# Performance work log

Measured on AMD Instinct MI355X. Metric: run time of the kernel, lower is better.

Reference implementation:

```python
import jax, jax.numpy as jnp
import numpy as np

B_IMG, T_PER, DIN = 8, 4096, 1176
D, E, BN, L, TOP_K, OUT = 1024, 8, 64, 4, 2, 4096


def setup_inputs() -> dict:
    key = jax.random.key(0)
    ks = jax.random.split(key, 16)
    s = 0.02
    inp = {
        "pixel_values": jax.random.normal(ks[0], (B_IMG * T_PER, DIN), jnp.float32),
        "image_grid_thw": jnp.tile(jnp.array([[1, 64, 64]], dtype=jnp.int64), (B_IMG, 1)),
        # in_proj (no bias)
        "w_in": jax.random.normal(ks[1], (DIN, D), jnp.float32) * s,
        # skin classifier: Linear(D,64) -> ReLU -> Linear(64,3)
        "w_sc1": jax.random.normal(ks[2], (D, 64), jnp.float32) * s,
        "b_sc1": jnp.zeros((64,), jnp.float32),
        "w_sc2": jax.random.normal(ks[3], (64, 3), jnp.float32) * s,
        "b_sc2": jnp.zeros((3,), jnp.float32),
        # per-adapter-layer routers (stacked over L)
        "w_rimg": jax.random.normal(ks[4], (L, D, E), jnp.float32) * s,
        "w_rskin": jax.random.normal(ks[5], (L, 3, E), jnp.float32) * s,
        # per-layer, per-expert MLP: Linear(D,BN) -> ReLU -> Linear(BN,D)
        "ew1": jax.random.normal(ks[6], (L, E, D, BN), jnp.float32) * s,
        "eb1": jnp.zeros((L, E, BN), jnp.float32),
        "ew2": jax.random.normal(ks[7], (L, E, BN, D), jnp.float32) * s,
        "eb2": jnp.zeros((L, E, D), jnp.float32),
        # out_proj
        "w_out": jax.random.normal(ks[8], (D, OUT), jnp.float32) * s,
        "b_out": jnp.zeros((OUT,), jnp.float32),
    }
    return inp


def _forward(pixel_values, image_grid_thw, w_in, w_sc1, b_sc1, w_sc2, b_sc2,
             w_rimg, w_rskin, ew1, eb1, ew2, eb2, w_out, b_out):
    B = image_grid_thw.shape[0]
    T = pixel_values.shape[0] // B  # equal chunk sizes (t*h*w identical per image)
    x = pixel_values.reshape(B, T, -1)

    def per_image(xc):  # xc: [T, din]
        h = xc @ w_in  # [T, D]
        g = h.mean(0)
        skin_logits = jax.nn.relu(g @ w_sc1 + b_sc1) @ w_sc2 + b_sc2  # [3]
        skin_probs = jax.nn.softmax(skin_logits)

        def layer(carry, params):
            h, aux = carry
            wri, wrs, W1, B1, W2, B2 = params
            logits = h @ wri + skin_probs @ wrs  # [T, E]
            probs = jax.nn.softmax(logits, axis=-1)
            tp, ti = jax.lax.top_k(probs, TOP_K)
            tp = tp / (tp.sum(-1, keepdims=True) + 1e-6)
            rows = jnp.arange(h.shape[0])[:, None]
            # dense per-token expert weights (0 for non-selected experts)
            wfull = jnp.zeros_like(probs).at[rows, ti].add(tp)
            mask = jnp.zeros_like(probs).at[rows, ti].add(1.0)
            h1 = jax.nn.relu(jnp.einsum('td,edb->teb', h, W1) + B1)  # [T,E,BN]
            h2 = jnp.einsum('teb,ebd->ted', h1, W2) + B2             # [T,E,D]
            moe_out = jnp.einsum('ted,te->td', h2, wfull)
            aux = aux + (probs.mean(0) * mask.mean(0)).sum() * probs.shape[-1]
            return (h + moe_out, aux), None

        (h, aux), _ = jax.lax.scan(layer, (h, jnp.zeros((), h.dtype)),
                                   (w_rimg, w_rskin, ew1, eb1, ew2, eb2))
        return h.mean(0), skin_logits, aux

    pooled, skin_logits, aux = jax.vmap(per_image)(x)
    vision_proj = pooled @ w_out + b_out
    return pooled, vision_proj, aux.sum(), skin_logits


def reference(pixel_values, image_grid_thw, w_in, w_sc1, b_sc1, w_sc2, b_sc2,
              w_rimg, w_rskin, ew1, eb1, ew2, eb2, w_out, b_out):
    return _forward(pixel_values, image_grid_thw, w_in, w_sc1, b_sc1, w_sc2, b_sc2,
                    w_rimg, w_rskin, ew1, eb1, ew2, eb2, w_out, b_out)
```

## Files before the change

### kernel.cpp

```cpp
#include <hip/hip_runtime.h>
#include <math.h>

#define TPI  4096
#define TT   32768
#define DIN  1176
#define KP   1216
#define DM   1024
#define NE   8
#define BN   64
#define NL   4
#define DOUT 4096

typedef __attribute__((ext_vector_type(4))) float floatx4;
typedef __attribute__((ext_vector_type(8))) short bf16x8;
typedef unsigned int uint;

__device__ inline short f2bf(float x) {
    unsigned u = __float_as_uint(x);
    u += 0x7fffu + ((u >> 16) & 1u);
    return (short)(u >> 16);
}
__device__ inline float bf2f(short h) {
    return __uint_as_float(((unsigned)(unsigned short)h) << 16);
}

#define GLP(p) ((const __attribute__((address_space(1))) void*)(p))
#define LDSP(p) ((__attribute__((address_space(3))) void*)(p))
#define ASYNC16(g, s) __builtin_amdgcn_global_load_lds(GLP(g), LDSP(s), 16, 0, 0)

#define OFF_H0    0ul
#define OFF_H1    67108864ul
#define OFF_XB    67108864ul
#define OFF_WBT   146800640ul
#define OFF_E1T   149291008ul
#define OFF_E2T   153485312ul
#define OFF_BTOK  157679616ul
#define OFF_BW1   157810688ul
#define OFF_BW2   157941760ul
#define OFF_T2E   158072832ul
#define OFF_T2W   158203904ul
#define OFF_Z     158466048ul
#define Z_BYTES   39232ul
#define OFF_RB    158505280ul
#define OFF_WRT   158506304ul

__global__ __launch_bounds__(256) void convx_kernel(
    const float* __restrict__ X, short* __restrict__ Xb)
{
    const long row = blockIdx.x;
    const float* src = X + row * (long)DIN;
    short* dst = Xb + row * (long)KP;
    for (int i = threadIdx.x; i < 304; i += 256) {
        short4 s;
        if (i < 294) {
            float4 v = *(const float4*)(src + i * 4);
            s.x = f2bf(v.x); s.y = f2bf(v.y); s.z = f2bf(v.z); s.w = f2bf(v.w);
        } else {
            s.x = 0; s.y = 0; s.z = 0; s.w = 0;
        }
        *(short4*)(dst + i * 4) = s;
    }
}

__global__ __launch_bounds__(256) void transp_kernel(
    const float* __restrict__ src, short* __restrict__ dst, int RS, int CS, int DK)
{
    __shared__ float tb[64][65];
    const int kt = blockIdx.x * 64, nt = blockIdx.y * 64;
    const long sb = (long)blockIdx.z * RS * CS;
    const long db = (long)blockIdx.z * CS * DK;
    const int rr = threadIdx.x >> 6, cc = threadIdx.x & 63;
#pragma unroll
    for (int i = 0; i < 16; ++i) {
        int r = i * 4 + rr;
        int k = kt + r, n = nt + cc;
        tb[r][cc] = (k < RS && n < CS) ? src[sb + (long)k * CS + n] : 0.0f;
    }
    __syncthreads();
#pragma unroll
    for (int i = 0; i < 16; ++i) {
        int r = i * 4 + rr;
        int n = nt + r, k = kt + cc;
        if (n < CS && k < DK) dst[db + (long)n * DK + k] = f2bf(tb[cc][r]);
    }
}

__global__ __launch_bounds__(256) void wrt_kernel(
    const float* __restrict__ w_rimg, short* __restrict__ wrT)
{
    const int l = blockIdx.x >> 4, e = blockIdx.x & 15;
    short* dst = wrT + ((long)l * 16 + e) * 1024;
    if (e < 8) {
        const float* src = w_rimg + (long)l * 8192 + e;
        for (int k = threadIdx.x; k < 1024; k += 256) dst[k] = f2bf(src[k * 8]);
    } else {
        for (int k = threadIdx.x; k < 1024; k += 256) dst[k] = 0;
    }
}

__global__ __launch_bounds__(256) void gemm_in_mfma(
    const short* __restrict__ Xb, const short* __restrict__ Wbt,
    short* __restrict__ Hb, float* __restrict__ g)
{
    __shared__ __align__(16) short As[128 * 64];
    __shared__ __align__(16) short Bs[128 * 64];
    const int tid = threadIdx.x;
    const int m0 = blockIdx.x * 128, n0 = blockIdx.y * 128;
    const int w = tid >> 6, lane = tid & 63;
    const int quad = lane >> 4, l15 = lane & 15;
    const int wm = (w >> 1) * 64, wn = (w & 1) * 64;

    floatx4 acc[4][4];
#pragma unroll
    for (int i = 0; i < 4; ++i)
#pragma unroll
        for (int j = 0; j < 4; ++j) acc[i][j] = 0.0f;

    const int r = tid >> 3;
    const int gofs = ((tid & 7) ^ (r & 7)) * 8;
    const short* ap = Xb + (long)(m0 + r) * KP + gofs;
    const short* bp = Wbt + (long)(n0 + r) * KP + gofs;
    short* asd = As + tid * 8;
    short* bsd = Bs + tid * 8;
    const int rx = l15 & 7;

    for (int k0 = 0; k0 < KP; k0 += 64) {
        __syncthreads();
#pragma unroll
        for (int i = 0; i < 4; ++i) {
            ASYNC16(ap + (long)i * 32 * KP + k0, asd + i * 2048);
            ASYNC16(bp + (long)i * 32 * KP + k0, bsd + i * 2048);
        }
        __syncthreads();
#pragma unroll
        for (int kk = 0; kk < 2; ++kk) {
            bf16x8 af[4], bfr[4];
#pragma unroll
            for (int i = 0; i < 4; ++i)
                af[i] = *(const bf16x8*)&As[(wm + i * 16 + l15) * 64 + (((kk * 4 + quad)) ^ rx) * 8];
#pragma unroll
            for (int j = 0; j < 4; ++j)
                bfr[j] = *(const bf16x8*)&Bs[(wn + j * 16 + l15) * 64 + (((kk * 4 + quad)) ^ rx) * 8];
#pragma unroll
            for (int i = 0; i < 4; ++i)
#pragma unroll
                for (int j = 0; j < 4; ++j)
                    acc[i][j] = __builtin_amdgcn_mfma_f32_16x16x32_bf16(af[i], bfr[j], acc[i][j], 0, 0, 0);
        }
    }
    const int img = m0 >> 12;
#pragma unroll
    for (int j = 0; j < 4; ++j) {
        float cs = 0.0f;
#pragma unroll
        for (int i = 0; i < 4; ++i)
#pragma unroll
            for (int r2 = 0; r2 < 4; ++r2) {
                short hv = f2bf(acc[i][j][r2]);
                Hb[(long)(m0 + wm + i * 16 + quad * 4 + r2) * DM + n0 + wn + j * 16 + l15] = hv;
                cs += bf2f(hv);
            }
        cs += __shfl_xor(cs, 16);
        cs += __shfl_xor(cs, 32);
        if (quad == 0)
            atomicAdd(&g[img * DM + n0 + wn + j * 16 + l15], cs * (1.0f / 4096.0f));
    }
}

__global__ __launch_bounds__(256) void colmean_kernel(
    const short* __restrict__ Hb, float* __restrict__ outp)
{
    const int col = blockIdx.x * 256 + threadIdx.x;
    const int img = blockIdx.y;
    const int t0 = blockIdx.z * 256;
    const short* p = Hb + ((long)img * TPI + t0) * DM + col;
    float s = 0.0f;
#pragma unroll 8
    for (int t = 0; t < 256; ++t) s += bf2f(p[(long)t * DM]);
    atomicAdd(&outp[img * DM + col], s * (1.0f / 4096.0f));
}

__global__ __launch_bounds__(256) void skin1_kernel(
    const float* __restrict__ g, const float* __restrict__ w_sc1,
    const float* __restrict__ b_sc1, float* __restrict__ hsg)
{
    __shared__ float red[4][64];
    const int img = blockIdx.x;
    const int part = threadIdx.x >> 6, c = threadIdx.x & 63;
    float s = 0.0f;
    for (int i = 0; i < 256; ++i) {
        int d = part * 256 + i;
        s += g[img * DM + d] * w_sc1[d * 64 + c];
    }
    red[part][c] = s;
    __syncthreads();
    if (part == 0) {
        float v = red[0][c] + red[1][c] + red[2][c] + red[3][c] + b_sc1[c];
        hsg[img * 64 + c] = fmaxf(v, 0.0f);
    }
}

__global__ __launch_bounds__(256) void skin2_kernel(
    const float* __restrict__ hsg, const float* __restrict__ w_sc2, const float* __restrict__ b_sc2,
    const float* __restrict__ w_rskin, float* __restrict__ skin_logits_out, float* __restrict__ rb)
{
    __shared__ float l3[24];
    __shared__ float sp[24];
    const int tid = threadIdx.x;
    if (tid < 24) {
        int img = tid / 3, j = tid % 3;
        float s = b_sc2[j];
        for (int c = 0; c < 64; ++c) s += hsg[img * 64 + c] * w_sc2[c * 3 + j];
        l3[tid] = s;
        skin_logits_out[tid] = s;
    }
    __syncthreads();
    if (tid < 8) {
        float v0 = l3[tid * 3], v1 = l3[tid * 3 + 1], v2 = l3[tid * 3 + 2];
        float m = fmaxf(v0, fmaxf(v1, v2));
        float e0 = expf(v0 - m), e1 = expf(v1 - m), e2 = expf(v2 - m);
        float inv = 1.0f / (e0 + e1 + e2);
        sp[tid * 3] = e0 * inv; sp[tid * 3 + 1] = e1 * inv; sp[tid * 3 + 2] = e2 * inv;
    }
    __syncthreads();
    {
        int l = tid >> 6, img = (tid >> 3) & 7, e = tid & 7;
        float s = 0.0f;
#pragma unroll
        for (int c = 0; c < 3; ++c) s += sp[img * 3 + c] * w_rskin[(l * 3 + c) * 8 + e];
        rb[tid] = s;
    }
}

__global__ __launch_bounds__(256) void router_kernel(
    const short* __restrict__ Hb, const short* __restrict__ wrT, const float* __restrict__ rb,
    uint* __restrict__ top2e, float* __restrict__ top2w, int* __restrict__ counts_pair,
    float* __restrict__ sum_probs, float* __restrict__ mask_cnt, int l)
{
    __shared__ __align__(16) short As[8 * 64 * 32];
    __shared__ float lgS[64 * 9];
    const int tid = threadIdx.x;
    const int tok0 = blockIdx.x * 64;
    const int img = tok0 >> 12;
    const int w = tid >> 6, lane = tid & 63;
    const int quad = lane >> 4, l15 = lane & 15;

    const short* rowptr = Hb + (long)(tok0 + w * 16 + (lane >> 2)) * DM + (lane & 3) * 8;
    short* sdst = As + tid * 8;
    const short* wrl = wrT + (long)l * 16 * 1024 + l15 * 1024 + quad * 8;

    floatx4 acc = 0.0f;
    for (int k0 = 0; k0 < DM; k0 += 256) {
        __syncthreads();
#pragma unroll
        for (int c = 0; c < 8; ++c) ASYNC16(rowptr + k0 + c * 32, sdst + c * 2048);
        __syncthreads();
#pragma unroll
        for (int c = 0; c < 8; ++c) {
            bf16x8 af = *(const bf16x8*)&As[c * 2048 + (w * 16 + l15) * 32 + quad * 8];
            bf16x8 bf = *(const bf16x8*)(wrl + k0 + c * 32);
            acc = __builtin_amdgcn_mfma_f32_16x16x32_bf16(af, bf, acc, 0, 0, 0);
        }
    }
    if (l15 < 8) {
#pragma unroll
        for (int r = 0; r < 4; ++r) lgS[(w * 16 + quad * 4 + r) * 9 + l15] = acc[r];
    }
    __syncthreads();

    if (tid < 64) {
        const int token = tok0 + tid;
        float p[8];
        float mx = -1e30f;
#pragma unroll
        for (int e = 0; e < 8; ++e) {
            float v = lgS[tid * 9 + e] + rb[l * 64 + img * 8 + e];
            p[e] = v; mx = fmaxf(mx, v);
        }
        float s = 0.0f;
#pragma unroll
        for (int e = 0; e < 8; ++e) { p[e] = expf(p[e] - mx); s += p[e]; }
        float inv = 1.0f / s;
#pragma unroll
        for (int e = 0; e < 8; ++e) p[e] *= inv;

        int i1 = 0; float b1v = p[0];
#pragma unroll
        for (int e = 1; e < 8; ++e) if (p[e] > b1v) { b1v = p[e]; i1 = e; }
        int i2 = -1; float b2v = -1.0f;
#pragma unroll
        for (int e = 0; e < 8; ++e) if (e != i1 && p[e] > b2v) { b2v = p[e]; i2 = e; }
        float den = b1v + b2v + 1e-6f;
        top2e[token] = (uint)i1 | ((uint)i2 << 8);
        top2w[2 * token] = b1v / den;
        top2w[2 * token + 1] = b2v / den;

        atomicAdd(&counts_pair[l * 64 + i1 * 8 + i2], 1);

        for (int slot = 0; slot < 2; ++slot) {
            int esel = slot ? i2 : i1;
#pragma unroll
            for (int e = 0; e < 8; ++e) {
                unsigned long long m = __ballot(esel == e);
                int pc = __popcll(m);
                if (pc && tid == (__ffsll(m) - 1))
                    atomicAdd(&mask_cnt[l * 64 + img * 8 + e], (float)pc);
            }
        }
#pragma unroll
        for (int e = 0; e < 8; ++e) {
            float rsum = p[e];
            for (int off = 32; off > 0; off >>= 1) rsum += __shfl_down(rsum, off);
            if (tid == 0) atomicAdd(&sum_probs[l * 64 + img * 8 + e], rsum);
        }
    }
}

__global__ __launch_bounds__(256) void scatter_kernel(
    const uint* __restrict__ top2e, const float* __restrict__ top2w,
    const int* __restrict__ counts_pair, int* __restrict__ cursors,
    int* __restrict__ btok, float* __restrict__ bw1, float* __restrict__ bw2, int l)
{
    __shared__ int pofS[64];
    const int tid = threadIdx.x;
    if (tid < 64) {
        int c = counts_pair[l * 64 + tid];
        int x = c;
#pragma unroll
        for (int off = 1; off < 64; off <<= 1) {
            int y = __shfl_up(x, off);
            if (tid >= off) x += y;
        }
        pofS[tid] = x - c;
    }
    __syncthreads();
    const int t = blockIdx.x * 256 + tid;
    const int lane = tid & 63;
    uint pe = top2e[t];
    int p = (int)(pe & 255u) * 8 + (int)((pe >> 8) & 255u);
    float w1 = top2w[2 * t], w2 = top2w[2 * t + 1];
    int myoff = pofS[p];
    unsigned long long rem = __ballot(true);
    while (rem) {
        int leader = __ffsll(rem) - 1;
        int pv = __shfl(p, leader);
        unsigned long long m = __ballot(p == pv);
        int basep = 0;
        if (lane == leader) basep = atomicAdd(&cursors[l * 64 + pv], __popcll(m));
        basep = __shfl(basep, leader);
        if (p == pv) {
            int pos = basep + __popcll(m & ((1ull << lane) - 1ull));
            int s = myoff + pos;
            btok[s] = t;
            bw1[s] = w1;
            bw2[s] = w2;
        }
        rem &= ~m;
    }
}

__global__ __launch_bounds__(256) void expert_pair(
    const short* __restrict__ Hin, short* __restrict__ Hout,
    int* __restrict__ counts_pair,
    const int* __restrict__ btok, const float* __restrict__ bw1, const float* __restrict__ bw2,
    const short* __restrict__ ew1t, const float* __restrict__ eb1,
    const short* __restrict__ ew2t, const float* __restrict__ eb2,
    const short* __restrict__ wrT, const float* __restrict__ rb,
    uint* __restrict__ top2e, float* __restrict__ top2w,
    float* __restrict__ sum_probs, float* __restrict__ mask_cnt, int l)
{
    __shared__ __align__(16) short As[8 * 64 * 32];
    __shared__ __align__(16) short h1a[64 * 72];
    __shared__ __align__(16) short h1b[64 * 72];
    __shared__ int tkS[64];
    __shared__ float w1S[64], w2S[64];
    __shared__ int pofS[64], cntS[64], tpS[64];
    __shared__ int nworkS;
    __shared__ float spLDS[64], mkLDS[64];

    const int tid = threadIdx.x;
    const int w = tid >> 6, lane = tid & 63;
    const int quad = lane >> 4, l15 = lane & 15;
    short* sdst = As + tid * 8;

    if (tid < 64) {
        int c = counts_pair[l * 64 + tid];
        cntS[tid] = c;
        int x = c;
#pragma unroll
        for (int off = 1; off < 64; off <<= 1) {
            int y = __shfl_up(x, off);
            if (tid >= off) x += y;
        }
        pofS[tid] = x - c;
        int nb = (c + 63) >> 6;
        int t = nb;
#pragma unroll
        for (int off = 1; off < 64; off <<= 1) {
            int y = __shfl_up(t, off);
            if (tid >= off) t += y;
        }
        tpS[tid] = t;
        if (tid == 63) nworkS = t;
    }
    __syncthreads();
    const int nwork = nworkS;

    for (int wi = blockIdx.x; wi < nwork; wi += gridDim.x) {
        int p = 0;
        while (p < 63 && tpS[p] <= wi) ++p;
        const int cnt = cntS[p];
        const int nbp = (cnt + 63) >> 6;
        const int base = (wi - (tpS[p] - nbp)) * 64;
        const int ea = p >> 3, eb = p & 7;
        const int off = pofS[p];

        __syncthreads();
        if (tid < 64) {
            bool valid = (base + tid) < cnt;
            int s = off + base + tid;
            tkS[tid] = valid ? btok[s] : 0;
            w1S[tid] = valid ? bw1[s] : 0.0f;
            w2S[tid] = valid ? bw2[s] : 0.0f;
            spLDS[tid] = 0.0f;
            mkLDS[tid] = 0.0f;
        }
        __syncthreads();
        const int lea = l * 8 + ea, leb = l * 8 + eb;
        const short* rowptr = Hin + (long)tkS[w * 16 + (lane >> 2)] * DM + (lane & 3) * 8;

        floatx4 acc1a[4], acc1b[4];
#pragma unroll
        for (int i = 0; i < 4; ++i) { acc1a[i] = 0.0f; acc1b[i] = 0.0f; }
        const short* w1ap = ew1t + ((long)lea * 64 + w * 16 + l15) * DM + quad * 8;
        const short* w1bp = ew1t + ((long)leb * 64 + w * 16 + l15) * DM + quad * 8;

        for (int k0 = 0; k0 < DM; k0 += 256) {
            __syncthreads();
#pragma unroll
            for (int c = 0; c < 8; ++c) ASYNC16(rowptr + k0 + c * 32, sdst + c * 2048);
            __syncthreads();
#pragma unroll
            for (int c = 0; c < 8; ++c) {
                bf16x8 ba = *(const bf16x8*)(w1ap + k0 + c * 32);
                bf16x8 bb = *(const bf16x8*)(w1bp + k0 + c * 32);
#pragma unroll
                for (int i = 0; i < 4; ++i) {
                    bf16x8 af = *(const bf16x8*)&As[c * 2048 + (i * 16 + l15) * 32 + quad * 8];
                    acc1a[i] = __builtin_amdgcn_mfma_f32_16x16x32_bf16(af, ba, acc1a[i], 0, 0, 0);
                    acc1b[i] = __builtin_amdgcn_mfma_f32_16x16x32_bf16(af, bb, acc1b[i], 0, 0, 0);
                }
            }
        }
        {
            float b1av = eb1[lea * BN + w * 16 + l15];
            float b1bv = eb1[leb * BN + w * 16 + l15];
#pragma unroll
            for (int i = 0; i < 4; ++i)
#pragma unroll
                for (int r = 0; r < 4; ++r) {
                    h1a[(i * 16 + quad * 4 + r) * 72 + w * 16 + l15] =
                        f2bf(fmaxf(acc1a[i][r] + b1av, 0.0f));
                    h1b[(i * 16 + quad * 4 + r) * 72 + w * 16 + l15] =
                        f2bf(fmaxf(acc1b[i][r] + b1bv, 0.0f));
                }
        }
        __syncthreads();

        const short* w2ap = ew2t + ((long)lea * DM + w * 16 + l15) * 64 + quad * 8;
        const short* w2bp = ew2t + ((long)leb * DM + w * 16 + l15) * 64 + quad * 8;
        const bool rowvalid = (base + (tid >> 2)) < cnt;
        const long orow = (long)tkS[tid >> 2] * DM;

        floatx4 acc_lg[4];
#pragma unroll
        for (int tf = 0; tf < 4; ++tf) acc_lg[tf] = 0.0f;

        for (int gidx = 0; gidx < 4; ++gidx) {
            const int g0 = gidx * 256;
#pragma unroll
            for (int c = 0; c < 8; ++c) ASYNC16(rowptr + g0 + c * 32, sdst + c * 2048);
            __syncthreads();
#pragma unroll
            for (int ns = 0; ns < 4; ++ns) {
                const int n0 = g0 + ns * 64;
                floatx4 a2a[4], a2b[4];
#pragma unroll
                for (int tj = 0; tj < 4; ++tj) { a2a[tj] = 0.0f; a2b[tj] = 0.0f; }
#pragma unroll
                for (int kk = 0; kk < 2; ++kk) {
                    bf16x8 wa = *(const bf16x8*)(w2ap + (long)n0 * 64 + kk * 32);
                    bf16x8 wb = *(const bf16x8*)(w2bp + (long)n0 * 64 + kk * 32);
#pragma unroll
                    for (int tj = 0; tj < 4; ++tj) {
                        bf16x8 ha = *(const bf16x8*)&h1a[(tj * 16 + l15) * 72 + kk * 32 + quad * 8];
                        bf16x8 hb = *(const bf16x8*)&h1b[(tj * 16 + l15) * 72 + kk * 32 + quad * 8];
                        a2a[tj] = __builtin_amdgcn_mfma_f32_16x16x32_bf16(wa, ha, a2a[tj], 0, 0, 0);
                        a2b[tj] = __builtin_amdgcn_mfma_f32_16x16x32_bf16(wb, hb, a2b[tj], 0, 0, 0);
                    }
                }
                const int nloc = ns * 64 + w * 16 + quad * 4;
                const int csub = nloc >> 5, cidx = nloc & 31;
                float4 b2av = *(const float4*)&eb2[lea * DM + g0 + nloc];
                float4 b2bv = *(const float4*)&eb2[leb * DM + g0 + nloc];
#pragma unroll
                for (int tj = 0; tj < 4; ++tj) {
                    int tk = tj * 16 + l15;
                    float w1 = w1S[tk], w2 = w2S[tk];
                    short* slot = &As[csub * 2048 + tk * 32 + cidx];
                    short4 res = *(short4*)slot;
                    short4 o;
                    o.x = f2bf(bf2f(res.x) + w1 * (a2a[tj][0] + b2av.x) + w2 * (a2b[tj][0] + b2bv.x));
                    o.y = f2bf(bf2f(res.y) + w1 * (a2a[tj][1] + b2av.y) + w2 * (a2b[tj][1] + b2bv.y));
                    o.z = f2bf(bf2f(res.z) + w1 * (a2a[tj][2] + b2av.z) + w2 * (a2b[tj][2] + b2bv.z));
                    o.w = f2bf(bf2f(res.w) + w1 * (a2a[tj][3] + b2av.w) + w2 * (a2b[tj][3] + b2bv.w));
                    *(short4*)slot = o;
                }
            }
            __syncthreads();

            if (l < 3) {
                const short* wrp = wrT + ((long)(l + 1) * 16 + l15) * 1024 + g0 + w * 64 + quad * 8;
#pragma unroll
                for (int kk = 0; kk < 2; ++kk) {
                    bf16x8 wf = *(const bf16x8*)(wrp + kk * 32);
#pragma unroll
                    for (int tf = 0; tf < 4; ++tf) {
                        bf16x8 of = *(const bf16x8*)&As[(w * 2 + kk) * 2048 + (tf * 16 + l15) * 32 + quad * 8];
                        acc_lg[tf] = __builtin_amdgcn_mfma_f32_16x16x32_bf16(wf, of, acc_lg[tf], 0, 0, 0);
                    }
                }
            }
            if (rowvalid) {
                const int tok = tid >> 2;
#pragma unroll
                for (int c2 = 0; c2 < 2; ++c2) {
                    const int csub = (tid & 3) * 2 + c2;
#pragma unroll
                    for (int j = 0; j < 4; ++j) {
                        int4 v = *(const int4*)&As[csub * 2048 + tok * 32 + j * 8];
                        *(int4*)(Hout + orow + g0 + csub * 32 + j * 8) = v;
                    }
                }
            }
            __syncthreads();
        }

        if (l < 3) {
            float* lgF = (float*)As;
#pragma unroll
            for (int tf = 0; tf < 4; ++tf)
                *(floatx4*)&lgF[(w * 64 + tf * 16 + l15) * 16 + quad * 4] = acc_lg[tf];
            __syncthreads();
            if (tid < 64) {
                const bool valid = (base + tid) < cnt;
                const int token = tkS[tid];
                const int img = token >> 12;
                float pb[8]; float mx = -1e30f;
#pragma unroll
                for (int e = 0; e < 8; ++e) {
                    float v = lgF[tid * 16 + e] + lgF[(64 + tid) * 16 + e]
                            + lgF[(128 + tid) * 16 + e] + lgF[(192 + tid) * 16 + e]
                            + rb[(l + 1) * 64 + img * 8 + e];
                    pb[e] = v; mx = fmaxf(mx, v);
                }
                float s = 0.0f;
#pragma unroll
                for (int e = 0; e < 8; ++e) { pb[e] = expf(pb[e] - mx); s += pb[e]; }
                float inv = 1.0f / s;
#pragma unroll
                for (int e = 0; e < 8; ++e) pb[e] *= inv;
                int i1 = 0; float b1v = pb[0];
#pragma unroll
                for (int e = 1; e < 8; ++e) if (pb[e] > b1v) { b1v = pb[e]; i1 = e; }
                int i2 = -1; float b2v = -1.0f;
#pragma unroll
                for (int e = 0; e < 8; ++e) if (e != i1 && pb[e] > b2v) { b2v = pb[e]; i2 = e; }
                if (valid) {
                    float den = b1v + b2v + 1e-6f;
                    top2e[token] = (uint)i1 | ((uint)i2 << 8);
                    top2w[2 * token] = b1v / den;
                    top2w[2 * token + 1] = b2v / den;
                    atomicAdd(&counts_pair[(l + 1) * 64 + i1 * 8 + i2], 1);
#pragma unroll
                    for (int e = 0; e < 8; ++e) atomicAdd(&spLDS[img * 8 + e], pb[e]);
                    atomicAdd(&mkLDS[img * 8 + i1], 1.0f);
                    atomicAdd(&mkLDS[img * 8 + i2], 1.0f);
                }
            }
            __syncthreads();
            if (tid < 64) {
                float v = spLDS[tid];
                if (v != 0.0f) atomicAdd(&sum_probs[(l + 1) * 64 + tid], v);
                float mz = mkLDS[tid];
                if (mz != 0.0f) atomicAdd(&mask_cnt[(l + 1) * 64 + tid], mz);
            }
        }
    }
}

__global__ __launch_bounds__(256) void vproj_kernel(
    const float* __restrict__ pooled, const float* __restrict__ w_out,
    const float* __restrict__ b_out, float* __restrict__ outp)
{
    __shared__ float ps[8 * 128];
    const int tid = threadIdx.x;
    const int n = blockIdx.x * 256 + tid;
    const int d0 = blockIdx.y * 128;
#pragma unroll
    for (int i = 0; i < 4; ++i) {
        int idx = tid + i * 256;
        ps[idx] = pooled[(idx >> 7) * DM + d0 + (idx & 127)];
    }
    __syncthreads();
    float acc[8];
    float binit = (blockIdx.y == 0) ? b_out[n] : 0.0f;
#pragma unroll
    for (int img = 0; img < 8; ++img) acc[img] = binit;
    for (int d = 0; d < 128; ++d) {
        float wv = w_out[(long)(d0 + d) * DOUT + n];
#pragma unroll
        for (int img = 0; img < 8; ++img) acc[img] += ps[img * 128 + d] * wv;
    }
#pragma unroll
    for (int img = 0; img < 8; ++img) atomicAdd(&outp[img * DOUT + n], acc[img]);
}

__global__ __launch_bounds__(64) void aux_kernel(
    const float* __restrict__ sum_probs, const float* __restrict__ mask_cnt,
    float* __restrict__ outp)
{
    const int tid = threadIdx.x;
    float v = 0.0f;
    if (tid < 32) {
        float s = 0.0f;
#pragma unroll
        for (int e = 0; e < 8; ++e) s += sum_probs[tid * 8 + e] * mask_cnt[tid * 8 + e];
        v = s * (8.0f / (4096.0f * 4096.0f));
    }
    for (int off = 32; off > 0; off >>= 1) v += __shfl_down(v, off);
    if (tid == 0) outp[0] = v;
}

extern "C" void kernel_launch(void* const* d_in, const int* in_sizes, int n_in,
                              void* d_out, int out_size, void* d_ws, size_t ws_size,
                              hipStream_t stream) {
    const float* X       = (const float*)d_in[0];
    const float* w_in    = (const float*)d_in[2];
    const float* w_sc1   = (const float*)d_in[3];
    const float* b_sc1   = (const float*)d_in[4];
    const float* w_sc2   = (const float*)d_in[5];
    const float* b_sc2   = (const float*)d_in[6];
    const float* w_rimg  = (const float*)d_in[7];
    const float* w_rskin = (const float*)d_in[8];
    const float* ew1     = (const float*)d_in[9];
    const float* eb1     = (const float*)d_in[10];
    const float* ew2     = (const float*)d_in[11];
    const float* eb2     = (const float*)d_in[12];
    const float* w_out   = (const float*)d_in[13];
    const float* b_out   = (const float*)d_in[14];

    float* out = (float*)d_out;
    char* ws = (char*)d_ws;

    short* H0   = (short*)(ws + OFF_H0);
    short* H1   = (short*)(ws + OFF_H1);
    short* Xb   = (short*)(ws + OFF_XB);
    short* Wbt  = (short*)(ws + OFF_WBT);
    short* ew1t = (short*)(ws + OFF_E1T);
    short* ew2t = (short*)(ws + OFF_E2T);
    int*   btok = (int*)(ws + OFF_BTOK);
    float* bw1  = (float*)(ws + OFF_BW1);
    float* bw2  = (float*)(ws + OFF_BW2);
    uint*  top2e = (uint*)(ws + OFF_T2E);
    float* top2w = (float*)(ws + OFF_T2W);
    int*   counts_pair = (int*)(ws + OFF_Z);
    int*   cursors     = (int*)(ws + OFF_Z + 1024);
    float* sum_probs   = (float*)(ws + OFF_Z + 2368);
    float* mask_cnt    = (float*)(ws + OFF_Z + 3392);
    float* g           = (float*)(ws + OFF_Z + 4416);
    float* hsg         = (float*)(ws + OFF_Z + 37184);
    float* rb          = (float*)(ws + OFF_RB);
    short* wrT         = (short*)(ws + OFF_WRT);

    hipMemsetAsync(d_out, 0, (size_t)out_size * sizeof(float), stream);
    hipMemsetAsync(ws + OFF_Z, 0, Z_BYTES, stream);

    dim3 b256(256);
    convx_kernel<<<TT, b256, 0, stream>>>(X, Xb);
    transp_kernel<<<dim3(19, 16, 1), b256, 0, stream>>>(w_in, Wbt, DIN, DM, KP);
    transp_kernel<<<dim3(16, 1, 32), b256, 0, stream>>>(ew1, ew1t, DM, BN, DM);
    transp_kernel<<<dim3(1, 16, 32), b256, 0, stream>>>(ew2, ew2t, BN, DM, BN);
    wrt_kernel<<<64, b256, 0, stream>>>(w_rimg, wrT);
    gemm_in_mfma<<<dim3(256, 8), b256, 0, stream>>>(Xb, Wbt, H0, g);
    skin1_kernel<<<8, b256, 0, stream>>>(g, w_sc1, b_sc1, hsg);
    skin2_kernel<<<1, b256, 0, stream>>>(hsg, w_sc2, b_sc2, w_rskin, out + 40961, rb);
    router_kernel<<<512, b256, 0, stream>>>(H0, wrT, rb, top2e, top2w,
                                            counts_pair, sum_probs, mask_cnt, 0);

    short* Hc = H0;
    short* Hn = H1;
    for (int l = 0; l < NL; ++l) {
        scatter_kernel<<<128, b256, 0, stream>>>(top2e, top2w, counts_pair, cursors,
                                                 btok, bw1, bw2, l);
        expert_pair<<<576, b256, 0, stream>>>(Hc, Hn, counts_pair, btok, bw1, bw2,
                                              ew1t, eb1, ew2t, eb2, wrT, rb,
                                              top2e, top2w, sum_probs, mask_cnt, l);
        short* tmp = Hc; Hc = Hn; Hn = tmp;
    }
    colmean_kernel<<<dim3(4, 8, 16), b256, 0, stream>>>(Hc, out);
    vproj_kernel<<<dim3(16, 8), b256, 0, stream>>>(out, w_out, b_out, out + 8192);
    aux_kernel<<<1, 64, 0, stream>>>(sum_probs, mask_cnt, out + 40960);
}
```

Before: 1.419 ms.

## Halve expert_pair token tile to 32 with swizzled LDS and more blocks

The expert-pair MoE kernel now processes 32 tokens per work item instead of 64. This shrinks the LDS footprint (a single XOR-swizzled row-major activation buffer, with the router logits aliased onto the h1 buffers) and the register accumulators, so more blocks can be resident (launch_bounds min 4) and the grid doubles to 1152. The h1 fragments are held in registers across the down-projection loop instead of being re-read from LDS. The trade-off is that each expert weight tile is reused across half as many tokens, so weight traffic per token roughly doubles, and padding waste per pair changes.

```diff
diff --git a/kernel.cpp b/kernel.cpp
--- a/kernel.cpp
+++ b/kernel.cpp
@@ -10,6 +10,7 @@
 #define BN   64
 #define NL   4
 #define DOUT 4096
+#define TBLK 32
 
 typedef __attribute__((ext_vector_type(4))) float floatx4;
 typedef __attribute__((ext_vector_type(8))) short bf16x8;
@@ -157,7 +158,8 @@
 #pragma unroll
             for (int r2 = 0; r2 < 4; ++r2) {
                 short hv = f2bf(acc[i][j][r2]);
-                Hb[(long)(m0 + wm + i * 16 + quad * 4 + r2) * DM + n0 + wn + j * 16 + l15] = hv;
+                Hb[(long)(m0 + wm + i * 16 + quad * 4 + r2) * DM + n0 + wn + j * 16 + l15] =
+                    hv;
                 cs += bf2f(hv);
             }
         cs += __shfl_xor(cs, 16);
@@ -359,7 +361,7 @@
     }
 }
 
-__global__ __launch_bounds__(256) void expert_pair(
+__global__ __launch_bounds__(256, 4) void expert_pair(
     const short* __restrict__ Hin, short* __restrict__ Hout,
     int* __restrict__ counts_pair,
     const int* __restrict__ btok, const float* __restrict__ bw1, const float* __restrict__ bw2,
@@ -369,19 +371,21 @@
     uint* __restrict__ top2e, float* __restrict__ top2w,
     float* __restrict__ sum_probs, float* __restrict__ mask_cnt, int l)
 {
-    __shared__ __align__(16) short As[8 * 64 * 32];
-    __shared__ __align__(16) short h1a[64 * 72];
-    __shared__ __align__(16) short h1b[64 * 72];
-    __shared__ int tkS[64];
-    __shared__ float w1S[64], w2S[64];
+    __shared__ __align__(16) short As[TBLK * 256];
+    __shared__ __align__(16) short h1ab[2][TBLK * 72];
+    __shared__ int tkS[TBLK];
+    __shared__ float w1S[TBLK], w2S[TBLK];
     __shared__ int pofS[64], cntS[64], tpS[64];
     __shared__ int nworkS;
     __shared__ float spLDS[64], mkLDS[64];
 
+    short* h1a = &h1ab[0][0];
+    short* h1b = &h1ab[1][0];
+    float* lgF = (float*)&h1ab[0][0];
+
     const int tid = threadIdx.x;
     const int w = tid >> 6, lane = tid & 63;
     const int quad = lane >> 4, l15 = lane & 15;
-    short* sdst = As + tid * 8;
 
     if (tid < 64) {
         int c = counts_pair[l * 64 + tid];
@@ -393,7 +397,7 @@
             if (tid >= off) x += y;
         }
         pofS[tid] = x - c;
-        int nb = (c + 63) >> 6;
+        int nb = (c + TBLK - 1) >> 5;
         int t = nb;
 #pragma unroll
         for (int off = 1; off < 64; off <<= 1) {
@@ -410,43 +414,49 @@
         int p = 0;
         while (p < 63 && tpS[p] <= wi) ++p;
         const int cnt = cntS[p];
-        const int nbp = (cnt + 63) >> 6;
-        const int base = (wi - (tpS[p] - nbp)) * 64;
+        const int nbp = (cnt + TBLK - 1) >> 5;
+        const int base = (wi - (tpS[p] - nbp)) * TBLK;
         const int ea = p >> 3, eb = p & 7;
         const int off = pofS[p];
+        const int lea = l * 8 + ea, leb = l * 8 + eb;
 
         __syncthreads();
-        if (tid < 64) {
+        if (tid < TBLK) {
             bool valid = (base + tid) < cnt;
             int s = off + base + tid;
             tkS[tid] = valid ? btok[s] : 0;
             w1S[tid] = valid ? bw1[s] : 0.0f;
             w2S[tid] = valid ? bw2[s] : 0.0f;
-            spLDS[tid] = 0.0f;
-            mkLDS[tid] = 0.0f;
-        }
+        }
+        if (tid < 64) { spLDS[tid] = 0.0f; mkLDS[tid] = 0.0f; }
         __syncthreads();
-        const int lea = l * 8 + ea, leb = l * 8 + eb;
-        const short* rowptr = Hin + (long)tkS[w * 16 + (lane >> 2)] * DM + (lane & 3) * 8;
-
-        floatx4 acc1a[4], acc1b[4];
-#pragma unroll
-        for (int i = 0; i < 4; ++i) { acc1a[i] = 0.0f; acc1b[i] = 0.0f; }
-        const short* w1ap = ew1t + ((long)lea * 64 + w * 16 + l15) * DM + quad * 8;
-        const short* w1bp = ew1t + ((long)leb * 64 + w * 16 + l15) * DM + quad * 8;
+
+        const int srow[4] = { tid >> 5, 8 + (tid >> 5), 16 + (tid >> 5), 24 + (tid >> 5) };
+        const int sj = tid & 31;
+
+        floatx4 acc1a[2], acc1b[2];
+#pragma unroll
+        for (int i = 0; i < 2; ++i) { acc1a[i] = 0.0f; acc1b[i] = 0.0f; }
+        const short* w1ap = ew1t + ((long)lea * BN + w * 16 + l15) * DM + quad * 8;
+        const short* w1bp = ew1t + ((long)leb * BN + w * 16 + l15) * DM + quad * 8;
 
         for (int k0 = 0; k0 < DM; k0 += 256) {
             __syncthreads();
 #pragma unroll
-            for (int c = 0; c < 8; ++c) ASYNC16(rowptr + k0 + c * 32, sdst + c * 2048);
+            for (int cc = 0; cc < 4; ++cc) {
+                const int row = srow[cc];
+                const short* src = Hin + (long)tkS[row] * DM + k0 + ((sj ^ (row & 7)) << 3);
+                ASYNC16(src, As + (cc * 256 + tid) * 8);
+            }
             __syncthreads();
 #pragma unroll
             for (int c = 0; c < 8; ++c) {
                 bf16x8 ba = *(const bf16x8*)(w1ap + k0 + c * 32);
                 bf16x8 bb = *(const bf16x8*)(w1bp + k0 + c * 32);
 #pragma unroll
-                for (int i = 0; i < 4; ++i) {
-                    bf16x8 af = *(const bf16x8*)&As[c * 2048 + (i * 16 + l15) * 32 + quad * 8];
+                for (int i = 0; i < 2; ++i) {
+                    const int tok = i * 16 + l15;
+                    bf16x8 af = *(const bf16x8*)&As[tok * 256 + (((c * 4 + quad) ^ (tok & 7)) << 3)];
                     acc1a[i] = __builtin_amdgcn_mfma_f32_16x16x32_bf16(af, ba, acc1a[i], 0, 0, 0);
                     acc1b[i] = __builtin_amdgcn_mfma_f32_16x16x32_bf16(af, bb, acc1b[i], 0, 0, 0);
                 }
@@ -456,7 +466,7 @@
             float b1av = eb1[lea * BN + w * 16 + l15];
             float b1bv = eb1[leb * BN + w * 16 + l15];
 #pragma unroll
-            for (int i = 0; i < 4; ++i)
+            for (int i = 0; i < 2; ++i)
 #pragma unroll
                 for (int r = 0; r < 4; ++r) {
                     h1a[(i * 16 + quad * 4 + r) * 72 + w * 16 + l15] =
@@ -467,100 +477,107 @@
         }
         __syncthreads();
 
+        bf16x8 hra[2][2], hrb[2][2];
+#pragma unroll
+        for (int kk = 0; kk < 2; ++kk)
+#pragma unroll
+            for (int tj = 0; tj < 2; ++tj) {
+                hra[kk][tj] = *(const bf16x8*)&h1a[(tj * 16 + l15) * 72 + kk * 32 + quad * 8];
+                hrb[kk][tj] = *(const bf16x8*)&h1b[(tj * 16 + l15) * 72 + kk * 32 + quad * 8];
+            }
+
         const short* w2ap = ew2t + ((long)lea * DM + w * 16 + l15) * 64 + quad * 8;
         const short* w2bp = ew2t + ((long)leb * DM + w * 16 + l15) * 64 + quad * 8;
-        const bool rowvalid = (base + (tid >> 2)) < cnt;
-        const long orow = (long)tkS[tid >> 2] * DM;
-
-        floatx4 acc_lg[4];
-#pragma unroll
-        for (int tf = 0; tf < 4; ++tf) acc_lg[tf] = 0.0f;
+        const short* wrp = wrT + ((long)(l + 1 < NL ? l + 1 : 0) * 16 + l15) * 1024 + quad * 8;
+
+        floatx4 acc_lg[2];
+#pragma unroll
+        for (int tf = 0; tf < 2; ++tf) acc_lg[tf] = 0.0f;
 
         for (int gidx = 0; gidx < 4; ++gidx) {
             const int g0 = gidx * 256;
-#pragma unroll
-            for (int c = 0; c < 8; ++c) ASYNC16(rowptr + g0 + c * 32, sdst + c * 2048);
+            __syncthreads();
+#pragma unroll
+            for (int cc = 0; cc < 4; ++cc) {
+                const int row = srow[cc];
+                const short* src = Hin + (long)tkS[row] * DM + g0 + ((sj ^ (row & 7)) << 3);
+                ASYNC16(src, As + (cc * 256 + tid) * 8);
+            }
             __syncthreads();
 #pragma unroll
             for (int ns = 0; ns < 4; ++ns) {
                 const int n0 = g0 + ns * 64;
-                floatx4 a2a[4], a2b[4];
-#pragma unroll
-                for (int tj = 0; tj < 4; ++tj) { a2a[tj] = 0.0f; a2b[tj] = 0.0f; }
+                floatx4 a2a[2], a2b[2];
+#pragma unroll
+                for (int tj = 0; tj < 2; ++tj) { a2a[tj] = 0.0f; a2b[tj] = 0.0f; }
 #pragma unroll
                 for (int kk = 0; kk < 2; ++kk) {
                     bf16x8 wa = *(const bf16x8*)(w2ap + (long)n0 * 64 + kk * 32);
                     bf16x8 wb = *(const bf16x8*)(w2bp + (long)n0 * 64 + kk * 32);
 #pragma unroll
-                    for (int tj = 0; tj < 4; ++tj) {
-                        bf16x8 ha = *(const bf16x8*)&h1a[(tj * 16 + l15) * 72 + kk * 32 + quad * 8];
-                        bf16x8 hb = *(const bf16x8*)&h1b[(tj * 16 + l15) * 72 + kk * 32 + quad * 8];
-                        a2a[tj] = __builtin_amdgcn_mfma_f32_16x16x32_bf16(wa, ha, a2a[tj], 0, 0, 0);
-                        a2b[tj] = __builtin_amdgcn_mfma_f32_16x16x32_bf16(wb, hb, a2b[tj], 0, 0, 0);
+                    for (int tj = 0; tj < 2; ++tj) {
+                        a2a[tj] = __builtin_amdgcn_mfma_f32_16x16x32_bf16(wa, hra[kk][tj], a2a[tj], 0, 0, 0);
+                        a2b[tj] = __builtin_amdgcn_mfma_f32_16x16x32_bf16(wb, hrb[kk][tj], a2b[tj], 0, 0, 0);
                     }
                 }
                 const int nloc = ns * 64 + w * 16 + quad * 4;
-                const int csub = nloc >> 5, cidx = nloc & 31;
+                const int jch = nloc >> 3, jof = nloc & 7;
                 float4 b2av = *(const float4*)&eb2[lea * DM + g0 + nloc];
                 float4 b2bv = *(const float4*)&eb2[leb * DM + g0 + nloc];
 #pragma unroll
-                for (int tj = 0; tj < 4; ++tj) {
+                for (int tj = 0; tj < 2; ++tj) {
                     int tk = tj * 16 + l15;
-                    float w1 = w1S[tk], w2 = w2S[tk];
-                    short* slot = &As[csub * 2048 + tk * 32 + cidx];
+                    float w1v = w1S[tk], w2v = w2S[tk];
+                    short* slot = &As[tk * 256 + ((jch ^ (tk & 7)) << 3) + jof];
                     short4 res = *(short4*)slot;
                     short4 o;
-                    o.x = f2bf(bf2f(res.x) + w1 * (a2a[tj][0] + b2av.x) + w2 * (a2b[tj][0] + b2bv.x));
-                    o.y = f2bf(bf2f(res.y) + w1 * (a2a[tj][1] + b2av.y) + w2 * (a2b[tj][1] + b2bv.y));
-                    o.z = f2bf(bf2f(res.z) + w1 * (a2a[tj][2] + b2av.z) + w2 * (a2b[tj][2] + b2bv.z));
-                    o.w = f2bf(bf2f(res.w) + w1 * (a2a[tj][3] + b2av.w) + w2 * (a2b[tj][3] + b2bv.w));
+                    o.x = f2bf(bf2f(res.x) + w1v * (a2a[tj][0] + b2av.x) + w2v * (a2b[tj][0] + b2bv.x));
+                    o.y = f2bf(bf2f(res.y) + w1v * (a2a[tj][1] + b2av.y) + w2v * (a2b[tj][1] + b2bv.y));
+                    o.z = f2bf(bf2f(res.z) + w1v * (a2a[tj][2] + b2av.z) + w2v * (a2b[tj][2] + b2bv.z));
+                    o.w = f2bf(bf2f(res.w) + w1v * (a2a[tj][3] + b2av.w) + w2v * (a2b[tj][3] + b2bv.w));
                     *(short4*)slot = o;
                 }
             }
             __syncthreads();
 
             if (l < 3) {
-                const short* wrp = wrT + ((long)(l + 1) * 16 + l15) * 1024 + g0 + w * 64 + quad * 8;
 #pragma unroll
                 for (int kk = 0; kk < 2; ++kk) {
-                    bf16x8 wf = *(const bf16x8*)(wrp + kk * 32);
-#pragma unroll
-                    for (int tf = 0; tf < 4; ++tf) {
-                        bf16x8 of = *(const bf16x8*)&As[(w * 2 + kk) * 2048 + (tf * 16 + l15) * 32 + quad * 8];
+                    const int c = w * 2 + kk;
+                    bf16x8 wf = *(const bf16x8*)(wrp + g0 + c * 32);
+#pragma unroll
+                    for (int tf = 0; tf < 2; ++tf) {
+                        const int tok = tf * 16 + l15;
+                        bf16x8 of = *(const bf16x8*)&As[tok * 256 + (((c * 4 + quad) ^ (tok & 7)) << 3)];
                         acc_lg[tf] = __builtin_amdgcn_mfma_f32_16x16x32_bf16(wf, of, acc_lg[tf], 0, 0, 0);
                     }
                 }
             }
-            if (rowvalid) {
-                const int tok = tid >> 2;
-#pragma unroll
-                for (int c2 = 0; c2 < 2; ++c2) {
-                    const int csub = (tid & 3) * 2 + c2;
-#pragma unroll
-                    for (int j = 0; j < 4; ++j) {
-                        int4 v = *(const int4*)&As[csub * 2048 + tok * 32 + j * 8];
-                        *(int4*)(Hout + orow + g0 + csub * 32 + j * 8) = v;
-                    }
+#pragma unroll
+            for (int cc = 0; cc < 4; ++cc) {
+                const int row = srow[cc];
+                if ((base + row) < cnt) {
+                    int4 v = *(const int4*)&As[row * 256 + ((sj ^ (row & 7)) << 3)];
+                    *(int4*)(Hout + (long)tkS[row] * DM + g0 + (sj << 3)) = v;
                 }
             }
+        }
+
+        if (l < 3) {
             __syncthreads();
-        }
-
-        if (l < 3) {
-            float* lgF = (float*)As;
-#pragma unroll
-            for (int tf = 0; tf < 4; ++tf)
-                *(floatx4*)&lgF[(w * 64 + tf * 16 + l15) * 16 + quad * 4] = acc_lg[tf];
+#pragma unroll
+            for (int tf = 0; tf < 2; ++tf)
+                *(floatx4*)&lgF[(w * 32 + tf * 16 + l15) * 16 + quad * 4] = acc_lg[tf];
             __syncthreads();
-            if (tid < 64) {
+            if (tid < TBLK) {
                 const bool valid = (base + tid) < cnt;
                 const int token = tkS[tid];
                 const int img = token >> 12;
                 float pb[8]; float mx = -1e30f;
 #pragma unroll
                 for (int e = 0; e < 8; ++e) {
-                    float v = lgF[tid * 16 + e] + lgF[(64 + tid) * 16 + e]
-                            + lgF[(128 + tid) * 16 + e] + lgF[(192 + tid) * 16 + e]
+                    float v = lgF[tid * 16 + e] + lgF[(32 + tid) * 16 + e]
+                            + lgF[(64 + tid) * 16 + e] + lgF[(96 + tid) * 16 + e]
                             + rb[(l + 1) * 64 + img * 8 + e];
                     pb[e] = v; mx = fmaxf(mx, v);
                 }
@@ -703,9 +720,9 @@
     for (int l = 0; l < NL; ++l) {
         scatter_kernel<<<128, b256, 0, stream>>>(top2e, top2w, counts_pair, cursors,
                                                  btok, bw1, bw2, l);
-        expert_pair<<<576, b256, 0, stream>>>(Hc, Hn, counts_pair, btok, bw1, bw2,
-                                              ew1t, eb1, ew2t, eb2, wrT, rb,
-                                              top2e, top2w, sum_probs, mask_cnt, l);
+        expert_pair<<<1152, b256, 0, stream>>>(Hc, Hn, counts_pair, btok, bw1, bw2,
+                                               ew1t, eb1, ew2t, eb2, wrT, rb,
+                                               top2e, top2w, sum_probs, mask_cnt, l);
         short* tmp = Hc; Hc = Hn; Hn = tmp;
     }
     colmean_kernel<<<dim3(4, 8, 16), b256, 0, stream>>>(Hc, out);
```

After: 1.525 ms. 1.07x slower.
